# Kernel optimization log

Measured on AMD Instinct MI355X. Metric: run time of the kernel, lower is better.

## Reference

```python
import jax, jax.numpy as jnp
import numpy as np

N, F_IN, H, L, E = 8192, 512, 256, 64, 262144


def gcn_conv(x, W, b, src, dst, dinv):
    # PyG GCNConv: out = D^{-1/2} (A + I) D^{-1/2} X W + b
    xw = x @ W                                   # [N, out]
    norm = dinv[src] * dinv[dst]                 # [E]
    agg = jax.ops.segment_sum(xw[src] * norm[:, None], dst, num_segments=x.shape[0])
    agg = agg + xw * (dinv * dinv)[:, None]      # self-loop contribution
    return agg + b


def setup_inputs() -> dict:
    key = jax.random.key(0)
    ks = jax.random.split(key, 9)
    x = jax.random.normal(ks[0], (N, F_IN), dtype=jnp.float32)
    edge_index = jax.random.randint(ks[1], (2, E), 0, N, dtype=jnp.int64)
    s = 1.0 / np.sqrt(F_IN)
    W1 = jax.random.uniform(ks[2], (F_IN, H), jnp.float32, -s, s)
    b1 = jnp.zeros((H,), jnp.float32)
    s2 = 1.0 / np.sqrt(H)
    Wmu = jax.random.uniform(ks[3], (H, L), jnp.float32, -s2, s2)
    bmu = jnp.zeros((L,), jnp.float32)
    Wsig = jax.random.uniform(ks[4], (H, L), jnp.float32, -s2, s2)
    bsig = jnp.zeros((L,), jnp.float32)
    gnoise = jax.random.normal(ks[5], (N, L), dtype=jnp.float32)
    return {"x": x, "edge_index": edge_index, "W1": W1, "b1": b1,
            "Wmu": Wmu, "bmu": bmu, "Wsig": Wsig, "bsig": bsig, "gnoise": gnoise}


def reference(x, edge_index, W1, b1, Wmu, bmu, Wsig, bsig, gnoise):
    src, dst = edge_index[0], edge_index[1]
    n = x.shape[0]
    # degree of A + I computed at target nodes (PyG default flow)
    deg = jax.ops.segment_sum(jnp.ones_like(src, dtype=x.dtype), dst, num_segments=n) + 1.0
    dinv = deg ** -0.5
    h = jax.nn.relu(gcn_conv(x, W1, b1, src, dst, dinv))
    # dropout is identity in eval mode
    xu = gcn_conv(h, Wmu, bmu, src, dst, dinv)   # mean head
    xs = gcn_conv(h, Wsig, bsig, src, dst, dinv)  # logstd head
    # NOTE: original forward calls decode(xs, xu) (arguments swapped),
    # so z = noise * exp(xu) + xs -- reproduced faithfully.
    z = gnoise * jnp.exp(xu) + xs                # [N, L]
    return jax.nn.sigmoid(z @ z.T)               # [N, N]
```

## Files before the change

### kernel.cpp

```cpp
#include <hip/hip_runtime.h>
#include <hip/hip_bf16.h>

#define NV 8192
#define FI 512
#define HD 256
#define LD 64
#define NE 262144

typedef __bf16 bf16x8 __attribute__((ext_vector_type(8)));
typedef float f32x4 __attribute__((ext_vector_type(4)));

__global__ void k_count(const int* __restrict__ ei, unsigned* __restrict__ deg) {
    int e = blockIdx.x * 256 + threadIdx.x;
    int d = ei[NE + e];
    atomicAdd(&deg[d], 1u);
}

__global__ void k_dinv(const unsigned* __restrict__ deg, float* __restrict__ dinv) {
    int i = blockIdx.x * 256 + threadIdx.x;
    dinv[i] = rsqrtf((float)(deg[i] + 1u));
}

__global__ void k_scan(const unsigned* __restrict__ cnt, unsigned* __restrict__ offs) {
    __shared__ unsigned sh[256];
    int tid = threadIdx.x;
    int base = tid * 32;
    unsigned local = 0;
    #pragma unroll
    for (int j = 0; j < 32; ++j) local += cnt[base + j];
    sh[tid] = local;
    __syncthreads();
    for (int off = 1; off < 256; off <<= 1) {
        unsigned v = 0;
        if (tid >= off) v = sh[tid - off];
        __syncthreads();
        if (tid >= off) sh[tid] += v;
        __syncthreads();
    }
    unsigned run = sh[tid] - local;
    for (int j = 0; j < 32; ++j) { offs[base + j] = run; run += cnt[base + j]; }
}

__global__ void k_scatter(const int* __restrict__ ei, const unsigned* __restrict__ offs,
                          unsigned* __restrict__ cur, const float* __restrict__ dinv,
                          int* __restrict__ srcs, float* __restrict__ normv) {
    int e = blockIdx.x * 256 + threadIdx.x;
    int s = ei[e], d = ei[NE + e];
    unsigned p = offs[d] + atomicAdd(&cur[d], 1u);
    srcs[p] = s;
    normv[p] = dinv[s] * dinv[d];
}

__global__ void k_split(const float* __restrict__ in, __bf16* __restrict__ hi,
                        __bf16* __restrict__ lo, int n) {
    int i = blockIdx.x * 256 + threadIdx.x;
    if (i < n) {
        float v = in[i];
        __bf16 h = (__bf16)v;
        hi[i] = h;
        lo[i] = (__bf16)(v - (float)h);
    }
}

__global__ void k_w1t_split(const float* __restrict__ W1, __bf16* __restrict__ hi,
                            __bf16* __restrict__ lo) {
    int idx = blockIdx.x * 256 + threadIdx.x;
    int h = idx >> 9, f = idx & (FI - 1);
    float v = W1[f * HD + h];
    __bf16 hh = (__bf16)v;
    hi[idx] = hh;
    lo[idx] = (__bf16)(v - (float)hh);
}

__global__ void k_wcat_split(const float* __restrict__ Wmu, const float* __restrict__ Wsig,
                             __bf16* __restrict__ hi, __bf16* __restrict__ lo) {
    int idx = blockIdx.x * 256 + threadIdx.x;
    int r = idx >> 8, k = idx & (HD - 1);
    float v = (r < LD) ? Wmu[k * LD + r] : Wsig[k * LD + (r - LD)];
    __bf16 hh = (__bf16)v;
    hi[idx] = hh;
    lo[idx] = (__bf16)(v - (float)hh);
}

template<int K, int NN_>
__global__ void k_gemm_split(const __bf16* __restrict__ Ah, const __bf16* __restrict__ Al,
                             const __bf16* __restrict__ Bh, const __bf16* __restrict__ Bl,
                             float* __restrict__ C) {
    int lane = threadIdx.x;
    int mi = blockIdx.x * 16, nj = blockIdx.y * 64;
    int la = lane & 15, kq = (lane >> 4) * 8;
    size_t arow = (size_t)(mi + la) * K + kq;
    f32x4 acc[4];
    #pragma unroll
    for (int t = 0; t < 4; ++t) acc[t] = (f32x4){0.f, 0.f, 0.f, 0.f};
    for (int k0 = 0; k0 < K; k0 += 32) {
        bf16x8 ah = *(const bf16x8*)(Ah + arow + k0);
        bf16x8 al = *(const bf16x8*)(Al + arow + k0);
        #pragma unroll
        for (int t = 0; t < 4; ++t) {
            size_t brow = (size_t)(nj + t * 16 + la) * K + kq + k0;
            bf16x8 bh = *(const bf16x8*)(Bh + brow);
            bf16x8 bl = *(const bf16x8*)(Bl + brow);
            acc[t] = __builtin_amdgcn_mfma_f32_16x16x32_bf16(ah, bh, acc[t], 0, 0, 0);
            acc[t] = __builtin_amdgcn_mfma_f32_16x16x32_bf16(ah, bl, acc[t], 0, 0, 0);
            acc[t] = __builtin_amdgcn_mfma_f32_16x16x32_bf16(al, bh, acc[t], 0, 0, 0);
        }
    }
    int rq = (lane >> 4) * 4;
    #pragma unroll
    for (int t = 0; t < 4; ++t)
        #pragma unroll
        for (int r = 0; r < 4; ++r)
            C[(size_t)(mi + rq + r) * NN_ + nj + t * 16 + la] = acc[t][r];
}

__global__ void k_agg1(const float* __restrict__ xw, const float* __restrict__ dinv,
                       const unsigned* __restrict__ offs, const unsigned* __restrict__ deg,
                       const int* __restrict__ srcs, const float* __restrict__ normv,
                       const float* __restrict__ b1, __bf16* __restrict__ hbh,
                       __bf16* __restrict__ hbl) {
    __shared__ int s_src[256];
    __shared__ float s_nrm[256];
    int d = blockIdx.x, f = threadIdx.x;
    float di = dinv[d];
    unsigned st = offs[d], cnt = deg[d];
    float s = xw[(size_t)d * HD + f] * di * di;
    for (unsigned b = 0; b < cnt; b += 256) {
        int nb = (int)min(256u, cnt - b);
        if (f < nb) { s_src[f] = srcs[st + b + f]; s_nrm[f] = normv[st + b + f]; }
        __syncthreads();
        for (int e = 0; e < nb; ++e)
            s += xw[(size_t)s_src[e] * HD + f] * s_nrm[e];
        __syncthreads();
    }
    s += b1[f];
    s = fmaxf(s, 0.f);
    __bf16 h = (__bf16)s;
    size_t o = (size_t)d * HD + f;
    hbh[o] = h;
    hbl[o] = (__bf16)(s - (float)h);
}

__global__ void k_agg2(const float* __restrict__ hw, const float* __restrict__ dinv,
                       const unsigned* __restrict__ offs, const unsigned* __restrict__ deg,
                       const int* __restrict__ srcs, const float* __restrict__ normv,
                       const float* __restrict__ bmu, const float* __restrict__ bsig,
                       const float* __restrict__ gno, __bf16* __restrict__ zh,
                       __bf16* __restrict__ zl) {
    __shared__ int s_src[128];
    __shared__ float s_nrm[128];
    __shared__ float sg[128];
    int d = blockIdx.x, f = threadIdx.x;
    float di = dinv[d];
    unsigned st = offs[d], cnt = deg[d];
    float s = hw[(size_t)d * 128 + f] * di * di;
    for (unsigned b = 0; b < cnt; b += 128) {
        int nb = (int)min(128u, cnt - b);
        if (f < nb) { s_src[f] = srcs[st + b + f]; s_nrm[f] = normv[st + b + f]; }
        __syncthreads();
        for (int e = 0; e < nb; ++e)
            s += hw[(size_t)s_src[e] * 128 + f] * s_nrm[e];
        __syncthreads();
    }
    s += (f < LD) ? bmu[f] : bsig[f - LD];
    sg[f] = s;
    __syncthreads();
    if (f < LD) {
        float xu = sg[f], xs = sg[LD + f];
        float z = gno[(size_t)d * LD + f] * __expf(xu) + xs;
        __bf16 h = (__bf16)z;
        size_t o = (size_t)d * LD + f;
        zh[o] = h;
        zl[o] = (__bf16)(z - (float)h);
    }
}

__launch_bounds__(256)
__global__ void k_zzt(const __bf16* __restrict__ Zh, const __bf16* __restrict__ Zl,
                      float* __restrict__ out) {
    __shared__ __bf16 zih[128][72], zil[128][72], zjh[128][72], zjl[128][72];
    int tid = threadIdx.x;
    int bi = blockIdx.x * 128, bj = blockIdx.y * 128;
    #pragma unroll
    for (int it = 0; it < 4; ++it) {
        int c = it * 256 + tid;
        int row = c >> 3, col = (c & 7) * 8;
        *(bf16x8*)&zih[row][col] = *(const bf16x8*)(Zh + (size_t)(bi + row) * LD + col);
        *(bf16x8*)&zil[row][col] = *(const bf16x8*)(Zl + (size_t)(bi + row) * LD + col);
        *(bf16x8*)&zjh[row][col] = *(const bf16x8*)(Zh + (size_t)(bj + row) * LD + col);
        *(bf16x8*)&zjl[row][col] = *(const bf16x8*)(Zl + (size_t)(bj + row) * LD + col);
    }
    __syncthreads();
    int wv = tid >> 6, lane = tid & 63;
    int m0 = wv * 32;
    int la = lane & 15, kq = (lane >> 4) * 8;
    f32x4 acc[2][8];
    #pragma unroll
    for (int s = 0; s < 2; ++s)
        #pragma unroll
        for (int t = 0; t < 8; ++t) acc[s][t] = (f32x4){0.f, 0.f, 0.f, 0.f};
    #pragma unroll
    for (int k0 = 0; k0 < LD; k0 += 32) {
        bf16x8 ah0 = *(const bf16x8*)&zih[m0 + la][k0 + kq];
        bf16x8 ah1 = *(const bf16x8*)&zih[m0 + 16 + la][k0 + kq];
        bf16x8 al0 = *(const bf16x8*)&zil[m0 + la][k0 + kq];
        bf16x8 al1 = *(const bf16x8*)&zil[m0 + 16 + la][k0 + kq];
        #pragma unroll
        for (int t = 0; t < 8; ++t) {
            bf16x8 bh = *(const bf16x8*)&zjh[t * 16 + la][k0 + kq];
            bf16x8 bl = *(const bf16x8*)&zjl[t * 16 + la][k0 + kq];
            acc[0][t] = __builtin_amdgcn_mfma_f32_16x16x32_bf16(ah0, bh, acc[0][t], 0, 0, 0);
            acc[0][t] = __builtin_amdgcn_mfma_f32_16x16x32_bf16(ah0, bl, acc[0][t], 0, 0, 0);
            acc[0][t] = __builtin_amdgcn_mfma_f32_16x16x32_bf16(al0, bh, acc[0][t], 0, 0, 0);
            acc[1][t] = __builtin_amdgcn_mfma_f32_16x16x32_bf16(ah1, bh, acc[1][t], 0, 0, 0);
            acc[1][t] = __builtin_amdgcn_mfma_f32_16x16x32_bf16(ah1, bl, acc[1][t], 0, 0, 0);
            acc[1][t] = __builtin_amdgcn_mfma_f32_16x16x32_bf16(al1, bh, acc[1][t], 0, 0, 0);
        }
    }
    int rq = (lane >> 4) * 4;
    #pragma unroll
    for (int s = 0; s < 2; ++s)
        #pragma unroll
        for (int t = 0; t < 8; ++t)
            #pragma unroll
            for (int r = 0; r < 4; ++r) {
                int row = bi + m0 + s * 16 + rq + r;
                int col = bj + t * 16 + la;
                float v = acc[s][t][r];
                out[(size_t)row * NV + col] = __builtin_amdgcn_rcpf(1.f + __expf(-v));
            }
}

extern "C" void kernel_launch(void* const* d_in, const int* in_sizes, int n_in,
                              void* d_out, int out_size, void* d_ws, size_t ws_size,
                              hipStream_t stream) {
    const float* x    = (const float*)d_in[0];
    const int*   ei   = (const int*)d_in[1];
    const float* W1   = (const float*)d_in[2];
    const float* b1   = (const float*)d_in[3];
    const float* Wmu  = (const float*)d_in[4];
    const float* bmu  = (const float*)d_in[5];
    const float* Wsig = (const float*)d_in[6];
    const float* bsig = (const float*)d_in[7];
    const float* gno  = (const float*)d_in[8];
    float* out = (float*)d_out;
    char* ws = (char*)d_ws;

    unsigned* deg   = (unsigned*)(ws + 0);
    unsigned* cur   = (unsigned*)(ws + 32768);
    unsigned* offs  = (unsigned*)(ws + 65536);
    float*    dinv  = (float*)   (ws + 98304);
    int*      srcs  = (int*)     (ws + 131072);
    float*    normv = (float*)   (ws + 1179648);
    __bf16*   w1th  = (__bf16*)  (ws + 2228224);
    __bf16*   w1tl  = (__bf16*)  (ws + 2490368);
    __bf16*   wch   = (__bf16*)  (ws + 2752512);
    __bf16*   wcl   = (__bf16*)  (ws + 2818048);
    char*     bufA  = ws + 2883584;
    char*     bufB  = ws + 19660800;
    __bf16* xh = (__bf16*)(bufA);
    __bf16* xl = (__bf16*)(bufA + 8388608);
    float*  xw = (float*)(bufB);
    __bf16* hbh = (__bf16*)(bufA);
    __bf16* hbl = (__bf16*)(bufA + 4194304);
    float*  hw  = (float*)(bufA + 8388608);
    __bf16* zh = (__bf16*)(bufB);
    __bf16* zl = (__bf16*)(bufB + 1048576);

    hipMemsetAsync(ws, 0, 65536, stream);
    k_count<<<NE / 256, 256, 0, stream>>>(ei, deg);
    k_dinv<<<NV / 256, 256, 0, stream>>>(deg, dinv);
    k_scan<<<1, 256, 0, stream>>>(deg, offs);
    k_scatter<<<NE / 256, 256, 0, stream>>>(ei, offs, cur, dinv, srcs, normv);
    k_split<<<(NV * FI) / 256, 256, 0, stream>>>(x, xh, xl, NV * FI);
    k_w1t_split<<<(HD * FI) / 256, 256, 0, stream>>>(W1, w1th, w1tl);
    k_wcat_split<<<(128 * HD) / 256, 256, 0, stream>>>(Wmu, Wsig, wch, wcl);
    k_gemm_split<FI, HD><<<dim3(NV / 16, HD / 64), 64, 0, stream>>>(xh, xl, w1th, w1tl, xw);
    k_agg1<<<NV, HD, 0, stream>>>(xw, dinv, offs, deg, srcs, normv, b1, hbh, hbl);
    k_gemm_split<HD, 128><<<dim3(NV / 16, 128 / 64), 64, 0, stream>>>(hbh, hbl, wch, wcl, hw);
    k_agg2<<<NV, 128, 0, stream>>>(hw, dinv, offs, deg, srcs, normv, bmu, bsig, gno, zh, zl);
    k_zzt<<<dim3(NV / 128, NV / 128), 256, 0, stream>>>(zh, zl, out);
}
```

Baseline: 437.2 us.

## Fuse prep kernels, store GEMM outputs as bf16, read zzt A-tile from global

```diff
diff --git a/kernel.cpp b/kernel.cpp
--- a/kernel.cpp
+++ b/kernel.cpp
@@ -10,24 +10,53 @@
 typedef __bf16 bf16x8 __attribute__((ext_vector_type(8)));
 typedef float f32x4 __attribute__((ext_vector_type(4)));
 
+__global__ void k_prep(const float* __restrict__ x, const float* __restrict__ W1,
+                       const float* __restrict__ Wmu, const float* __restrict__ Wsig,
+                       __bf16* __restrict__ xh, __bf16* __restrict__ xl,
+                       __bf16* __restrict__ w1th, __bf16* __restrict__ w1tl,
+                       __bf16* __restrict__ wch, __bf16* __restrict__ wcl,
+                       unsigned* __restrict__ deg, unsigned* __restrict__ cur) {
+    int idx = blockIdx.x * 256 + threadIdx.x;
+    if (idx < 2 * NV) {
+        if (idx < NV) deg[idx] = 0u; else cur[idx - NV] = 0u;
+    }
+    if (idx < NV * FI) {
+        float v = x[idx];
+        __bf16 h = (__bf16)v;
+        xh[idx] = h;
+        xl[idx] = (__bf16)(v - (float)h);
+    } else if (idx < NV * FI + HD * FI) {
+        int j = idx - NV * FI;
+        int h = j >> 9, f = j & (FI - 1);
+        float v = W1[f * HD + h];
+        __bf16 b = (__bf16)v;
+        w1th[j] = b;
+        w1tl[j] = (__bf16)(v - (float)b);
+    } else if (idx < NV * FI + HD * FI + 128 * HD) {
+        int j = idx - NV * FI - HD * FI;
+        int r = j >> 8, k = j & (HD - 1);
+        float v = (r < LD) ? Wmu[k * LD + r] : Wsig[k * LD + (r - LD)];
+        __bf16 b = (__bf16)v;
+        wch[j] = b;
+        wcl[j] = (__bf16)(v - (float)b);
+    }
+}
+
 __global__ void k_count(const int* __restrict__ ei, unsigned* __restrict__ deg) {
     int e = blockIdx.x * 256 + threadIdx.x;
     int d = ei[NE + e];
     atomicAdd(&deg[d], 1u);
 }
 
-__global__ void k_dinv(const unsigned* __restrict__ deg, float* __restrict__ dinv) {
-    int i = blockIdx.x * 256 + threadIdx.x;
-    dinv[i] = rsqrtf((float)(deg[i] + 1u));
-}
-
-__global__ void k_scan(const unsigned* __restrict__ cnt, unsigned* __restrict__ offs) {
+__global__ void k_scan(const unsigned* __restrict__ cnt, unsigned* __restrict__ offs,
+                       float* __restrict__ dinv) {
     __shared__ unsigned sh[256];
     int tid = threadIdx.x;
     int base = tid * 32;
+    unsigned c[32];
     unsigned local = 0;
     #pragma unroll
-    for (int j = 0; j < 32; ++j) local += cnt[base + j];
+    for (int j = 0; j < 32; ++j) { c[j] = cnt[base + j]; local += c[j]; }
     sh[tid] = local;
     __syncthreads();
     for (int off = 1; off < 256; off <<= 1) {
@@ -38,7 +67,12 @@
         __syncthreads();
     }
     unsigned run = sh[tid] - local;
-    for (int j = 0; j < 32; ++j) { offs[base + j] = run; run += cnt[base + j]; }
+    #pragma unroll
+    for (int j = 0; j < 32; ++j) {
+        offs[base + j] = run;
+        dinv[base + j] = rsqrtf((float)(c[j] + 1u));
+        run += c[j];
+    }
 }
 
 __global__ void k_scatter(const int* __restrict__ ei, const unsigned* __restrict__ offs,
@@ -51,41 +85,10 @@
     normv[p] = dinv[s] * dinv[d];
 }
 
-__global__ void k_split(const float* __restrict__ in, __bf16* __restrict__ hi,
-                        __bf16* __restrict__ lo, int n) {
-    int i = blockIdx.x * 256 + threadIdx.x;
-    if (i < n) {
-        float v = in[i];
-        __bf16 h = (__bf16)v;
-        hi[i] = h;
-        lo[i] = (__bf16)(v - (float)h);
-    }
-}
-
-__global__ void k_w1t_split(const float* __restrict__ W1, __bf16* __restrict__ hi,
-                            __bf16* __restrict__ lo) {
-    int idx = blockIdx.x * 256 + threadIdx.x;
-    int h = idx >> 9, f = idx & (FI - 1);
-    float v = W1[f * HD + h];
-    __bf16 hh = (__bf16)v;
-    hi[idx] = hh;
-    lo[idx] = (__bf16)(v - (float)hh);
-}
-
-__global__ void k_wcat_split(const float* __restrict__ Wmu, const float* __restrict__ Wsig,
-                             __bf16* __restrict__ hi, __bf16* __restrict__ lo) {
-    int idx = blockIdx.x * 256 + threadIdx.x;
-    int r = idx >> 8, k = idx & (HD - 1);
-    float v = (r < LD) ? Wmu[k * LD + r] : Wsig[k * LD + (r - LD)];
-    __bf16 hh = (__bf16)v;
-    hi[idx] = hh;
-    lo[idx] = (__bf16)(v - (float)hh);
-}
-
 template<int K, int NN_>
 __global__ void k_gemm_split(const __bf16* __restrict__ Ah, const __bf16* __restrict__ Al,
                              const __bf16* __restrict__ Bh, const __bf16* __restrict__ Bl,
-                             float* __restrict__ C) {
+                             __bf16* __restrict__ C) {
     int lane = threadIdx.x;
     int mi = blockIdx.x * 16, nj = blockIdx.y * 64;
     int la = lane & 15, kq = (lane >> 4) * 8;
@@ -111,10 +114,10 @@
     for (int t = 0; t < 4; ++t)
         #pragma unroll
         for (int r = 0; r < 4; ++r)
-            C[(size_t)(mi + rq + r) * NN_ + nj + t * 16 + la] = acc[t][r];
-}
-
-__global__ void k_agg1(const float* __restrict__ xw, const float* __restrict__ dinv,
+            C[(size_t)(mi + rq + r) * NN_ + nj + t * 16 + la] = (__bf16)acc[t][r];
+}
+
+__global__ void k_agg1(const __bf16* __restrict__ xwb, const float* __restrict__ dinv,
                        const unsigned* __restrict__ offs, const unsigned* __restrict__ deg,
                        const int* __restrict__ srcs, const float* __restrict__ normv,
                        const float* __restrict__ b1, __bf16* __restrict__ hbh,
@@ -124,13 +127,13 @@
     int d = blockIdx.x, f = threadIdx.x;
     float di = dinv[d];
     unsigned st = offs[d], cnt = deg[d];
-    float s = xw[(size_t)d * HD + f] * di * di;
+    float s = (float)xwb[(size_t)d * HD + f] * di * di;
     for (unsigned b = 0; b < cnt; b += 256) {
         int nb = (int)min(256u, cnt - b);
         if (f < nb) { s_src[f] = srcs[st + b + f]; s_nrm[f] = normv[st + b + f]; }
         __syncthreads();
         for (int e = 0; e < nb; ++e)
-            s += xw[(size_t)s_src[e] * HD + f] * s_nrm[e];
+            s += (float)xwb[(size_t)s_src[e] * HD + f] * s_nrm[e];
         __syncthreads();
     }
     s += b1[f];
@@ -141,7 +144,7 @@
     hbl[o] = (__bf16)(s - (float)h);
 }
 
-__global__ void k_agg2(const float* __restrict__ hw, const float* __restrict__ dinv,
+__global__ void k_agg2(const __bf16* __restrict__ hwb, const float* __restrict__ dinv,
                        const unsigned* __restrict__ offs, const unsigned* __restrict__ deg,
                        const int* __restrict__ srcs, const float* __restrict__ normv,
                        const float* __restrict__ bmu, const float* __restrict__ bsig,
@@ -153,13 +156,13 @@
     int d = blockIdx.x, f = threadIdx.x;
     float di = dinv[d];
     unsigned st = offs[d], cnt = deg[d];
-    float s = hw[(size_t)d * 128 + f] * di * di;
+    float s = (float)hwb[(size_t)d * 128 + f] * di * di;
     for (unsigned b = 0; b < cnt; b += 128) {
         int nb = (int)min(128u, cnt - b);
         if (f < nb) { s_src[f] = srcs[st + b + f]; s_nrm[f] = normv[st + b + f]; }
         __syncthreads();
         for (int e = 0; e < nb; ++e)
-            s += hw[(size_t)s_src[e] * 128 + f] * s_nrm[e];
+            s += (float)hwb[(size_t)s_src[e] * 128 + f] * s_nrm[e];
         __syncthreads();
     }
     s += (f < LD) ? bmu[f] : bsig[f - LD];
@@ -178,15 +181,13 @@
 __launch_bounds__(256)
 __global__ void k_zzt(const __bf16* __restrict__ Zh, const __bf16* __restrict__ Zl,
                       float* __restrict__ out) {
-    __shared__ __bf16 zih[128][72], zil[128][72], zjh[128][72], zjl[128][72];
+    __shared__ __bf16 zjh[128][72], zjl[128][72];
     int tid = threadIdx.x;
     int bi = blockIdx.x * 128, bj = blockIdx.y * 128;
     #pragma unroll
     for (int it = 0; it < 4; ++it) {
         int c = it * 256 + tid;
         int row = c >> 3, col = (c & 7) * 8;
-        *(bf16x8*)&zih[row][col] = *(const bf16x8*)(Zh + (size_t)(bi + row) * LD + col);
-        *(bf16x8*)&zil[row][col] = *(const bf16x8*)(Zl + (size_t)(bi + row) * LD + col);
         *(bf16x8*)&zjh[row][col] = *(const bf16x8*)(Zh + (size_t)(bj + row) * LD + col);
         *(bf16x8*)&zjl[row][col] = *(const bf16x8*)(Zl + (size_t)(bj + row) * LD + col);
     }
@@ -201,10 +202,12 @@
         for (int t = 0; t < 8; ++t) acc[s][t] = (f32x4){0.f, 0.f, 0.f, 0.f};
     #pragma unroll
     for (int k0 = 0; k0 < LD; k0 += 32) {
-        bf16x8 ah0 = *(const bf16x8*)&zih[m0 + la][k0 + kq];
-        bf16x8 ah1 = *(const bf16x8*)&zih[m0 + 16 + la][k0 + kq];
-        bf16x8 al0 = *(const bf16x8*)&zil[m0 + la][k0 + kq];
-        bf16x8 al1 = *(const bf16x8*)&zil[m0 + 16 + la][k0 + kq];
+        size_t r0 = (size_t)(bi + m0 + la) * LD + k0 + kq;
+        size_t r1 = (size_t)(bi + m0 + 16 + la) * LD + k0 + kq;
+        bf16x8 ah0 = *(const bf16x8*)(Zh + r0);
+        bf16x8 al0 = *(const bf16x8*)(Zl + r0);
+        bf16x8 ah1 = *(const bf16x8*)(Zh + r1);
+        bf16x8 al1 = *(const bf16x8*)(Zl + r1);
         #pragma unroll
         for (int t = 0; t < 8; ++t) {
             bf16x8 bh = *(const bf16x8*)&zjh[t * 16 + la][k0 + kq];
@@ -258,26 +261,24 @@
     __bf16*   wcl   = (__bf16*)  (ws + 2818048);
     char*     bufA  = ws + 2883584;
     char*     bufB  = ws + 19660800;
-    __bf16* xh = (__bf16*)(bufA);
-    __bf16* xl = (__bf16*)(bufA + 8388608);
-    float*  xw = (float*)(bufB);
+    __bf16* xh  = (__bf16*)(bufA);
+    __bf16* xl  = (__bf16*)(bufA + 8388608);
+    __bf16* xwb = (__bf16*)(bufB);
     __bf16* hbh = (__bf16*)(bufA);
     __bf16* hbl = (__bf16*)(bufA + 4194304);
-    float*  hw  = (float*)(bufA + 8388608);
+    __bf16* hwb = (__bf16*)(bufA + 8388608);
     __bf16* zh = (__bf16*)(bufB);
     __bf16* zl = (__bf16*)(bufB + 1048576);
 
-    hipMemsetAsync(ws, 0, 65536, stream);
+    const int prep_elems = NV * FI + HD * FI + 128 * HD;
+    k_prep<<<prep_elems / 256, 256, 0, stream>>>(x, W1, Wmu, Wsig, xh, xl, w1th, w1tl,
+                                                 wch, wcl, deg, cur);
     k_count<<<NE / 256, 256, 0, stream>>>(ei, deg);
-    k_dinv<<<NV / 256, 256, 0, stream>>>(deg, dinv);
-    k_scan<<<1, 256, 0, stream>>>(deg, offs);
+    k_scan<<<1, 256, 0, stream>>>(deg, offs, dinv);
     k_scatter<<<NE / 256, 256, 0, stream>>>(ei, offs, cur, dinv, srcs, normv);
-    k_split<<<(NV * FI) / 256, 256, 0, stream>>>(x, xh, xl, NV * FI);
-    k_w1t_split<<<(HD * FI) / 256, 256, 0, stream>>>(W1, w1th, w1tl);
-    k_wcat_split<<<(128 * HD) / 256, 256, 0, stream>>>(Wmu, Wsig, wch, wcl);
-    k_gemm_split<FI, HD><<<dim3(NV / 16, HD / 64), 64, 0, stream>>>(xh, xl, w1th, w1tl, xw);
-    k_agg1<<<NV, HD, 0, stream>>>(xw, dinv, offs, deg, srcs, normv, b1, hbh, hbl);
-    k_gemm_split<HD, 128><<<dim3(NV / 16, 128 / 64), 64, 0, stream>>>(hbh, hbl, wch, wcl, hw);
-    k_agg2<<<NV, 128, 0, stream>>>(hw, dinv, offs, deg, srcs, normv, bmu, bsig, gno, zh, zl);
+    k_gemm_split<FI, HD><<<dim3(NV / 16, HD / 64), 64, 0, stream>>>(xh, xl, w1th, w1tl, xwb);
+    k_agg1<<<NV, HD, 0, stream>>>(xwb, dinv, offs, deg, srcs, normv, b1, hbh, hbl);
+    k_gemm_split<HD, 128><<<dim3(NV / 16, 128 / 64), 64, 0, stream>>>(hbh, hbl, wch, wcl, hwb);
+    k_agg2<<<NV, 128, 0, stream>>>(hwb, dinv, offs, deg, srcs, normv, bmu, bsig, gno, zh, zl);
     k_zzt<<<dim3(NV / 128, NV / 128), 256, 0, stream>>>(zh, zl, out);
 }
```

Measured after the change: 432.8 us. About the same (-1.0%).
